# Kernel tuning notes

Measured on AMD Instinct MI355X. Metric: run time of the kernel, lower is better.

The kernel has to match this reference:

```python
import jax, jax.numpy as jnp
import numpy as np

B, N, D = 4, 2048, 1024
H = 8
DK = D // H            # 128, head qk dim (pre feature map)
DV = D // H            # 128, head v dim
DF = 2 * DK            # 256, hedgehog feature dim
CHUNK = 64
RMS_EPS = 1e-5


def setup_inputs() -> dict:
    key = jax.random.key(0)
    ks = jax.random.split(key, 10)
    s = D ** -0.5
    x = jax.random.normal(ks[0], (B, N, D), dtype=jnp.float32)
    Wq = jax.random.normal(ks[1], (D, D), dtype=jnp.float32) * s
    Wk = jax.random.normal(ks[2], (D, D), dtype=jnp.float32) * s
    Wv = jax.random.normal(ks[3], (D, D), dtype=jnp.float32) * s
    Wo = jax.random.normal(ks[4], (D, D), dtype=jnp.float32) * s
    eye = jnp.eye(DK, dtype=jnp.float32)
    # Hedgehog maps are initialized as identity; add small noise to exercise math
    fmq_w = eye + 0.02 * jax.random.normal(ks[5], (DK, DK), dtype=jnp.float32)
    fmq_b = 0.02 * jax.random.normal(ks[6], (DK,), dtype=jnp.float32)
    fmk_w = eye + 0.02 * jax.random.normal(ks[7], (DK, DK), dtype=jnp.float32)
    fmk_b = 0.02 * jax.random.normal(ks[8], (DK,), dtype=jnp.float32)
    rms_w = 1.0 + 0.1 * jax.random.normal(ks[9], (DV,), dtype=jnp.float32)
    return {"x": x, "Wq": Wq, "Wk": Wk, "Wv": Wv, "Wo": Wo,
            "fmq_w": fmq_w, "fmq_b": fmq_b, "fmk_w": fmk_w, "fmk_b": fmk_b,
            "rms_w": rms_w}


def _hedgehog(x, w, b):
    # x: [B,H,N,DK]; Linear then concat(exp(y), exp(-y)) -> [B,H,N,2*DK]
    y = jnp.einsum('bhnd,ed->bhne', x, w) + b
    return jnp.concatenate([jnp.exp(y), jnp.exp(-y)], axis=-1)


def _fused_chunk_linear_attn(q, k, v):
    # Causal linear attention via chunked recurrence.
    # q,k: [B,H,N,DF]; v: [B,H,N,DV]; q already scaled.
    b, h, n, df = q.shape
    dv = v.shape[-1]
    nc = n // CHUNK
    def to_chunks(t):
        d = t.shape[-1]
        return t.reshape(b, h, nc, CHUNK, d).transpose(2, 0, 1, 3, 4)  # [Nc,B,H,C,d]
    qc, kc, vc = to_chunks(q), to_chunks(k), to_chunks(v)
    mask = jnp.tril(jnp.ones((CHUNK, CHUNK), dtype=bool))

    def step(S, inp):
        qi, ki, vi = inp                                   # [B,H,C,*]
        attn = jnp.einsum('bhcd,bhed->bhce', qi, ki)       # intra-chunk scores
        attn = jnp.where(mask, attn, 0.0)                  # causal (inclusive)
        intra = jnp.einsum('bhce,bhev->bhcv', attn, vi)
        inter = jnp.einsum('bhcd,bhdv->bhcv', qi, S)       # past-chunk state
        S = S + jnp.einsum('bhcd,bhcv->bhdv', ki, vi)
        return S, intra + inter

    S0 = jnp.zeros((b, h, df, dv), dtype=q.dtype)
    _, oc = jax.lax.scan(step, S0, (qc, kc, vc))           # oc: [Nc,B,H,C,DV]
    return oc.transpose(1, 2, 0, 3, 4).reshape(b, h, n, dv)


def reference(x, Wq, Wk, Wv, Wo, fmq_w, fmq_b, fmk_w, fmk_b, rms_w):
    b, n, d = x.shape
    split = lambda t: t.reshape(b, n, H, -1).transpose(0, 2, 1, 3)  # b h n d
    q = split(x @ Wq.T)
    k = split(x @ Wk.T)
    v = split(x @ Wv.T)
    q = _hedgehog(q, fmq_w, fmq_b)          # [B,H,N,DF]
    k = _hedgehog(k, fmk_w, fmk_b)
    scale = q.shape[-1] ** -0.5             # fla default: feat_dim**-0.5
    o = _fused_chunk_linear_attn(q * scale, k, v)
    # RMSNorm over head_v_dim
    o = o * jax.lax.rsqrt(jnp.mean(o * o, axis=-1, keepdims=True) + RMS_EPS) * rms_w
    o = o.transpose(0, 2, 1, 3).reshape(b, n, H * DV)
    return o @ Wo.T
```

## Files before the change

### kernel.cpp

```cpp
#include <hip/hip_runtime.h>
#include <cstdint>
#include <cstddef>

#define DEV __device__ __forceinline__

typedef __attribute__((ext_vector_type(8))) short   short8;
typedef __attribute__((ext_vector_type(4))) short   sshort4;
typedef __attribute__((ext_vector_type(8))) __bf16  bf16x8;
typedef __attribute__((ext_vector_type(4))) float   f32x4;

typedef void as1_void __attribute__((address_space(1)));
typedef void as3_void __attribute__((address_space(3)));

DEV short f2b(float f) {
  unsigned u = __float_as_uint(f);
  unsigned r = (u + 0x7fffu + ((u >> 16) & 1u)) >> 16;
  return (short)r;
}
DEV float b2f(short s) {
  return __uint_as_float(((unsigned)(unsigned short)s) << 16);
}

DEV void gload16(const void* g, void* l) {
  __builtin_amdgcn_global_load_lds((as1_void*)g, (as3_void*)l, 16, 0, 0);
}

DEV bf16x8 ld8(const short* p) { return *reinterpret_cast<const bf16x8*>(p); }

DEV f32x4 mfma16(bf16x8 a, bf16x8 b, f32x4 c) {
  return __builtin_amdgcn_mfma_f32_16x16x32_bf16(a, b, c, 0, 0, 0);
}

__global__ void convert_kernel(const float* __restrict__ src, short* __restrict__ dst, int n) {
  int i = (blockIdx.x * 256 + threadIdx.x) * 8;
  if (i + 8 > n) return;
  float4 a = *(const float4*)(src + i);
  float4 b = *(const float4*)(src + i + 4);
  short8 o;
  o[0] = f2b(a.x); o[1] = f2b(a.y); o[2] = f2b(a.z); o[3] = f2b(a.w);
  o[4] = f2b(b.x); o[5] = f2b(b.y); o[6] = f2b(b.z); o[7] = f2b(b.w);
  *(short8*)(dst + i) = o;
}

__global__ void eff_weights2_kernel(const float* __restrict__ Wq, const float* __restrict__ Wk,
                                    const float* __restrict__ fmq_w, const float* __restrict__ fmk_w,
                                    short* __restrict__ Wcat)
{
  __shared__ float fm[16 * 128];
  const int blk = blockIdx.x;
  const int sel = blk >> 6, h = (blk >> 3) & 7, eg = blk & 7;
  const float* W   = sel ? Wk : Wq;
  const float* fmw = sel ? fmk_w : fmq_w;
  const int tid = threadIdx.x;
  const int e0 = eg * 16;
  for (int i = tid; i < 2048; i += 256) fm[i] = fmw[e0 * 128 + i];
  __syncthreads();
  float acc[16][4] = {};
  for (int d = 0; d < 128; d += 4) {
    f32x4 w0 = *(const f32x4*)(W + (size_t)(h * 128 + d + 0) * 1024 + tid * 4);
    f32x4 w1 = *(const f32x4*)(W + (size_t)(h * 128 + d + 1) * 1024 + tid * 4);
    f32x4 w2 = *(const f32x4*)(W + (size_t)(h * 128 + d + 2) * 1024 + tid * 4);
    f32x4 w3 = *(const f32x4*)(W + (size_t)(h * 128 + d + 3) * 1024 + tid * 4);
#pragma unroll
    for (int e = 0; e < 16; ++e) {
      f32x4 fv = *(const f32x4*)&fm[e * 128 + d];
#pragma unroll
      for (int c = 0; c < 4; ++c)
        acc[e][c] += fv[0] * w0[c] + fv[1] * w1[c] + fv[2] * w2[c] + fv[3] * w3[c];
    }
  }
#pragma unroll
  for (int e = 0; e < 16; ++e) {
    sshort4 o;
#pragma unroll
    for (int c = 0; c < 4; ++c) o[c] = f2b(acc[e][c]);
    *(sshort4*)(Wcat + (size_t)(sel * 1024 + h * 128 + e0 + e) * 1024 + tid * 4) = o;
  }
}

template<int EPI>
__launch_bounds__(512, 2)
__global__ void gemm256(const short* __restrict__ A, const short* __restrict__ B,
                        const int K, const int N, float* __restrict__ C,
                        const float* __restrict__ qb, const float* __restrict__ kb,
                        short* __restrict__ qf, short* __restrict__ kf,
                        short* __restrict__ kfT, short* __restrict__ vT)
{
  __shared__ __align__(16) short lds[65536];
  float* ep = (float*)lds;

  const int tid = threadIdx.x;
  const int w = tid >> 6, l = tid & 63;
  const int wr = w >> 2, wc = w & 3;

  const int nbx = gridDim.x;
  const int orig = blockIdx.y * nbx + blockIdx.x;
  const int cpx = (nbx * gridDim.y) >> 3;
  const int wg = (orig & 7) * cpx + (orig >> 3);
  const int m0 = (wg / nbx) * 256, n0 = (wg % nbx) * 256;

  const int srow = tid >> 3;
  const int scol = ((tid & 7) ^ (srow & 7)) * 8;
  const int wbase = w * 8;

  f32x4 acc[8][4] = {};

  auto STG = [&](const short* src, int g0, int p, int aoff, int R, int t) {
    gload16(src + (size_t)(g0 + R + srow) * K + t * 64 + scol,
            lds + p * 32768 + aoff + (R + wbase) * 64);
  };

#pragma unroll
  for (int R = 0; R < 256; R += 64) {
    STG(A, m0, 0, 0, R, 0);
    STG(B, n0, 0, 16384, R, 0);
    STG(A, m0, 1, 0, R, 1);
    STG(B, n0, 1, 16384, R, 1);
  }
  asm volatile("s_waitcnt vmcnt(0)" ::: "memory");
  __builtin_amdgcn_s_barrier();

#define PHASE(p, q, STAGES, TAIL) { \
    bf16x8 af[4][2], bf[2][2]; \
    _Pragma("unroll") \
    for (int m = 0; m < 4; ++m) { \
      const int r = wr * 128 + ((q) >> 1) * 64 + m * 16 + (l & 15); \
      _Pragma("unroll") \
      for (int kk = 0; kk < 2; ++kk) \
        af[m][kk] = ld8(lds + (p) * 32768 + r * 64 + ((kk * 4 + (l >> 4)) ^ (r & 7)) * 8); \
    } \
    _Pragma("unroll") \
    for (int n = 0; n < 2; ++n) { \
      const int r = wc * 64 + ((q) & 1) * 32 + n * 16 + (l & 15); \
      _Pragma("unroll") \
      for (int kk = 0; kk < 2; ++kk) \
        bf[n][kk] = ld8(lds + (p) * 32768 + 16384 + r * 64 + ((kk * 4 + (l >> 4)) ^ (r & 7)) * 8); \
    } \
    STAGES; \
    __builtin_amdgcn_s_barrier(); \
    asm volatile("s_waitcnt lgkmcnt(0)" ::: "memory"); \
    __builtin_amdgcn_sched_barrier(0); \
    __builtin_amdgcn_s_setprio(1); \
    _Pragma("unroll") \
    for (int m = 0; m < 4; ++m) \
      _Pragma("unroll") \
      for (int n = 0; n < 2; ++n) \
        _Pragma("unroll") \
        for (int kk = 0; kk < 2; ++kk) \
          acc[((q) >> 1) * 4 + m][((q) & 1) * 2 + n] = \
            mfma16(af[m][kk], bf[n][kk], acc[((q) >> 1) * 4 + m][((q) & 1) * 2 + n]); \
    __builtin_amdgcn_s_setprio(0); \
    TAIL; \
    __builtin_amdgcn_s_barrier(); \
  }

  const int NI = K >> 7;
  for (int i = 0; i < NI; ++i) {
    const int t1 = 2 * i + 1, t2 = 2 * i + 2, t3 = 2 * i + 3;
    const bool sE = (i < NI - 1), sL = (i > 0);
    PHASE(0, 0, {
      if (sL) { STG(A, m0, 1, 0, 64, t1); STG(A, m0, 1, 0, 192, t1);
                STG(B, n0, 1, 16384, 0, t1); STG(B, n0, 1, 16384, 64, t1); } }, {});
    PHASE(0, 1, {
      if (sL) { STG(B, n0, 1, 16384, 128, t1); STG(B, n0, 1, 16384, 192, t1); } }, {});
    PHASE(0, 2, {
      if (sE) { STG(A, m0, 0, 0, 0, t2); STG(A, m0, 0, 0, 128, t2); } }, {});
    PHASE(0, 3, {}, {
      if (i == NI - 1) { asm volatile("s_waitcnt vmcnt(0)" ::: "memory"); }
      else             { asm volatile("s_waitcnt vmcnt(2)" ::: "memory"); } });
    PHASE(1, 0, {
      if (sE) { STG(A, m0, 0, 0, 64, t2); STG(A, m0, 0, 0, 192, t2); } }, {});
    PHASE(1, 1, {
      if (sE) { STG(B, n0, 0, 16384, 0, t2); STG(B, n0, 0, 16384, 64, t2); } }, {});
    PHASE(1, 2, {
      if (sE) { STG(B, n0, 0, 16384, 128, t2); STG(B, n0, 0, 16384, 192, t2); } }, {});
    PHASE(1, 3, {
      if (sE) { STG(A, m0, 1, 0, 0, t3); STG(A, m0, 1, 0, 128, t3); } }, {
      asm volatile("s_waitcnt vmcnt(2)" ::: "memory"); });
  }
#undef PHASE

  const int seg = (EPI == 1) ? (n0 >> 10) : 0;
  const int b = m0 >> 11, tok0 = m0 & 2047, c0 = tok0 >> 6;
  const int hbase = (n0 & 1023) >> 7;
  const int bh0 = b * 8 + hbase;

#pragma unroll
  for (int h = 0; h < 4; ++h) {
    __syncthreads();
    if (wr == (h >> 1)) {
      const int mbase = (h & 1) * 4;
#pragma unroll
      for (int n = 0; n < 4; ++n) {
        const int cl = wc * 64 + n * 16 + (l & 15);
        float bb = 0.f;
        if constexpr (EPI == 1) bb = (seg == 0) ? qb[cl & 127] : (seg == 1) ? kb[cl & 127] : 0.f;
#pragma unroll
        for (int m4 = 0; m4 < 4; ++m4)
#pragma unroll
          for (int r = 0; r < 4; ++r) {
            const int rl = m4 * 16 + (l >> 4) * 4 + r;
            ep[rl * 264 + (cl ^ ((rl & 3) << 2))] = acc[mbase + m4][n][r] + bb;
          }
      }
    }
    __syncthreads();

    if constexpr (EPI == 0) {
#pragma unroll
      for (int it = 0; it < 8; ++it) {
        const int tl = it * 8 + (tid >> 6);
        const int cc4 = (tid & 63) * 4;
        f32x4 v4 = *(const f32x4*)&ep[tl * 264 + (cc4 ^ ((tl & 3) << 2))];
        *(f32x4*)(C + (size_t)(m0 + h * 64 + tl) * N + n0 + cc4) = v4;
      }
    } else {
      const int cc = c0 + h;
      if (seg <= 1) {
        short* dst = (seg == 0) ? qf : kf;
        const float sc = (seg == 0) ? 0.0625f : 1.0f;
#pragma unroll
        for (int it = 0; it < 8; ++it) {
          const int tl = it * 8 + (tid >> 6);
          const int cc4 = (tid & 63) * 4;
          f32x4 y4 = *(const f32x4*)&ep[tl * 264 + (cc4 ^ ((tl & 3) << 2))];
          sshort4 sp, sm;
#pragma unroll
          for (int j = 0; j < 4; ++j) {
            sp[j] = f2b(__expf(y4[j]) * sc);
            sm[j] = f2b(__expf(-y4[j]) * sc);
          }
          const int hh = cc4 >> 7, e = cc4 & 127;
          short* rowp = dst + ((size_t)(bh0 + hh) * 2048 + tok0 + h * 64 + tl) * 256;
          *(sshort4*)(rowp + e)       = sp;
          *(sshort4*)(rowp + 128 + e) = sm;
        }
        if (seg == 1) {
#pragma unroll
          for (int p2 = 0; p2 < 8; ++p2) {
            const int idx = p2 * 512 + tid;
            const int er = idx >> 3, oct = (idx & 7) * 8;
            const int hh = er >> 8, rr = er & 255, e = rr & 127, sg = rr >> 7;
            const int cgc = hh * 128 + e;
            short8 o;
#pragma unroll
            for (int ii = 0; ii < 8; ++ii) {
              float y = ep[(oct + ii) * 264 + (cgc ^ (((oct + ii) & 3) << 2))];
              o[ii] = f2b(__expf(sg ? -y : y));
            }
            *(short8*)(kfT + ((size_t)(bh0 + hh) * 32 + cc) * 16384 + (size_t)rr * 64 + oct) = o;
          }
        }
      } else {
#pragma unroll
        for (int p2 = 0; p2 < 4; ++p2) {
          const int idx = p2 * 512 + tid;
          const int er = idx >> 3, oct = (idx & 7) * 8;
          const int hh = er >> 7, vv = er & 127;
          short8 o;
#pragma unroll
          for (int ii = 0; ii < 8; ++ii)
            o[ii] = f2b(ep[(oct + ii) * 264 + (er ^ (((oct + ii) & 3) << 2))]);
          *(short8*)(vT + ((size_t)(bh0 + hh) * 32 + cc) * 8192 + (size_t)vv * 64 + oct) = o;
        }
      }
    }
  }
}

__launch_bounds__(256, 3)
__global__ void passA_kernel(const short* __restrict__ kfT, const short* __restrict__ vT,
                             short* __restrict__ GT)
{
  const int bhc = blockIdx.x;
  const int tid = threadIdx.x, w = tid >> 6, l = tid & 63;
  __shared__ __align__(16) short skT[256 * 64];
  __shared__ __align__(16) short svt[128 * 64];
  const short* kg = kfT + (size_t)bhc * 256 * 64;
  const short* vg = vT  + (size_t)bhc * 128 * 64;
  short* G = GT + (size_t)bhc * 128 * 256;
  const int sr8 = l >> 3, sl8 = ((l & 7) ^ sr8) * 8;

#pragma unroll
  for (int j = 0; j < 8; ++j) {
    const int seg = w * 8 + j;
    gload16(kg + (size_t)(seg * 8 + sr8) * 64 + sl8, skT + seg * 512);
  }
#pragma unroll
  for (int j = 0; j < 4; ++j) {
    const int seg = w * 4 + j;
    gload16(vg + (size_t)(seg * 8 + sr8) * 64 + sl8, svt + seg * 512);
  }
  __syncthreads();

#pragma unroll
  for (int mi = 0; mi < 2; ++mi) {
    const int v0 = w * 32 + mi * 16;
    bf16x8 a[2];
#pragma unroll
    for (int ks = 0; ks < 2; ++ks)
      a[ks] = ld8(svt + (v0 + (l & 15)) * 64 + ((ks * 4 + (l >> 4)) ^ (l & 7)) * 8);
    f32x4 acc[16] = {};
#pragma unroll
    for (int nt = 0; nt < 16; ++nt)
#pragma unroll
      for (int ks = 0; ks < 2; ++ks) {
        bf16x8 b = ld8(skT + (nt * 16 + (l & 15)) * 64 + ((ks * 4 + (l >> 4)) ^ (l & 7)) * 8);
        acc[nt] = mfma16(a[ks], b, acc[nt]);
      }
#pragma unroll
    for (int nt = 0; nt < 16; ++nt)
#pragma unroll
      for (int r = 0; r < 4; ++r)
        G[(v0 + (l >> 4) * 4 + r) * 256 + nt * 16 + (l & 15)] = f2b(acc[nt][r]);
  }
}

__global__ void prefix_kernel(short* __restrict__ GT) {
  const int bh = blockIdx.x >> 4, slab = blockIdx.x & 15;
  short* base = GT + (size_t)bh * 32 * 32768 + slab * 2048 + threadIdx.x * 8;
  float acc[8] = {};
  short8 g = *(const short8*)base;
  for (int c = 0; c < 32; ++c) {
    short* p = base + (size_t)c * 32768;
    short8 gn = {};
    if (c < 31) gn = *(const short8*)(p + 32768);
    short8 s;
#pragma unroll
    for (int j = 0; j < 8; ++j) s[j] = f2b(acc[j]);
    *(short8*)p = s;
#pragma unroll
    for (int j = 0; j < 8; ++j) acc[j] += b2f(g[j]);
    g = gn;
  }
}

__launch_bounds__(256, 3)
__global__ void passC_kernel(const short* __restrict__ qf, const short* __restrict__ kf,
                             const short* __restrict__ vT, const short* __restrict__ ST,
                             const float* __restrict__ rms_w, short* __restrict__ o_n)
{
  const int bhc = blockIdx.x, bh = bhc >> 5, c = bhc & 31;
  const int tid = threadIdx.x, w = tid >> 6, l = tid & 63;
  __shared__ __align__(16) short bufA[64 * 256];
  __shared__ __align__(16) short bufV[64 * 64];
  __shared__ __align__(16) short attn[64 * 72];
  const short* qg = qf + ((size_t)bh * 2048 + c * 64) * 256;
  const short* kg = kf + ((size_t)bh * 2048 + c * 64) * 256;
  const short* vg = vT + (size_t)bhc * 128 * 64;
  const short* sg = ST + (size_t)bhc * 128 * 256;
  const int r0 = w * 16;
  const int sr8 = l >> 3, sl8 = ((l & 7) ^ sr8) * 8;
  const int l5 = l >> 5, s32 = l & 31;

#pragma unroll
  for (int j = 0; j < 8; ++j) {
    const int seg = w * 8 + j;
    const int row = seg * 2 + l5;
    gload16(kg + (size_t)row * 256 + (s32 ^ (row & 7)) * 8, bufA + seg * 512);
  }
  bf16x8 qreg[8];
#pragma unroll
  for (int ks = 0; ks < 8; ++ks)
    qreg[ks] = ld8(qg + (size_t)(r0 + (l & 15)) * 256 + ks * 32 + (l >> 4) * 8);

  __syncthreads();
  f32x4 s[4] = {};
#pragma unroll
  for (int ks = 0; ks < 8; ++ks) {
    const int rs = ((ks * 4 + (l >> 4)) ^ (l & 7)) * 8;
#pragma unroll
    for (int nt = 0; nt < 4; ++nt)
      s[nt] = mfma16(qreg[ks], ld8(bufA + (nt * 16 + (l & 15)) * 256 + rs), s[nt]);
  }
#pragma unroll
  for (int nt = 0; nt < 4; ++nt)
#pragma unroll
    for (int r = 0; r < 4; ++r) {
      int rr = r0 + (l >> 4) * 4 + r;
      int tt = nt * 16 + (l & 15);
      attn[rr * 72 + tt] = (tt <= rr) ? f2b(s[nt][r]) : (short)0;
    }

  f32x4 o[8] = {};
#pragma unroll
  for (int h = 0; h < 2; ++h) {
    __syncthreads();
#pragma unroll
    for (int j = 0; j < 8; ++j) {
      const int seg = w * 8 + j;
      const int row = seg * 2 + l5;
      gload16(sg + (size_t)(h * 64 + row) * 256 + (s32 ^ (row & 7)) * 8, bufA + seg * 512);
    }
#pragma unroll
    for (int j = 0; j < 2; ++j) {
      const int seg = w * 2 + j;
      const int row = seg * 8 + sr8;
      gload16(vg + (size_t)(h * 64 + row) * 64 + sl8, bufV + seg * 512);
    }
    __syncthreads();
#pragma unroll
    for (int ks = 0; ks < 2; ++ks) {
      bf16x8 a = ld8(attn + (r0 + (l & 15)) * 72 + ks * 32 + (l >> 4) * 8);
      const int rs = ((ks * 4 + (l >> 4)) ^ (l & 7)) * 8;
#pragma unroll
      for (int nt = 0; nt < 4; ++nt)
        o[h * 4 + nt] = mfma16(a, ld8(bufV + (nt * 16 + (l & 15)) * 64 + rs), o[h * 4 + nt]);
    }
#pragma unroll
    for (int ks = 0; ks < 8; ++ks) {
      const int rs = ((ks * 4 + (l >> 4)) ^ (l & 7)) * 8;
#pragma unroll
      for (int nt = 0; nt < 4; ++nt)
        o[h * 4 + nt] = mfma16(qreg[ks], ld8(bufA + (nt * 16 + (l & 15)) * 256 + rs), o[h * 4 + nt]);
    }
  }

  const int b = bh >> 3, hh = bh & 7;
#pragma unroll
  for (int r = 0; r < 4; ++r) {
    float ss = 0.f;
#pragma unroll
    for (int nt = 0; nt < 8; ++nt) ss += o[nt][r] * o[nt][r];
    ss += __shfl_xor(ss, 1);
    ss += __shfl_xor(ss, 2);
    ss += __shfl_xor(ss, 4);
    ss += __shfl_xor(ss, 8);
    float sc = rsqrtf(ss * (1.0f / 128.0f) + 1e-5f);
    int tok = c * 64 + r0 + (l >> 4) * 4 + r;
    size_t ob = ((size_t)b * 2048 + tok) * 1024 + hh * 128;
#pragma unroll
    for (int nt = 0; nt < 8; ++nt) {
      int vcol = nt * 16 + (l & 15);
      o_n[ob + vcol] = f2b(o[nt][r] * sc * rms_w[vcol]);
    }
  }
}

extern "C" void kernel_launch(void* const* d_in, const int* in_sizes, int n_in,
                              void* d_out, int out_size, void* d_ws, size_t ws_size,
                              hipStream_t stream)
{
  const float* x     = (const float*)d_in[0];
  const float* Wq    = (const float*)d_in[1];
  const float* Wk    = (const float*)d_in[2];
  const float* Wv    = (const float*)d_in[3];
  const float* Wo    = (const float*)d_in[4];
  const float* fmq_w = (const float*)d_in[5];
  const float* fmq_b = (const float*)d_in[6];
  const float* fmk_w = (const float*)d_in[7];
  const float* fmk_b = (const float*)d_in[8];
  const float* rms_w = (const float*)d_in[9];
  float* out = (float*)d_out;

  char* ws = (char*)d_ws;
  short* x_b  = (short*)(ws);
  short* Wcat = (short*)(ws + 16777216);
  short* Wo_b = (short*)(ws + 23068672);
  short* qf   = (short*)(ws + 25165824);
  short* kf   = (short*)(ws + 58720256);
  short* kfT  = (short*)(ws + 92274688);
  short* vT   = (short*)(ws + 125829120);
  short* GT   = (short*)(ws + 142606336);
  short* o_n  = x_b;

  convert_kernel<<<4096, 256, 0, stream>>>(x, x_b, 8388608);
  convert_kernel<<<512, 256, 0, stream>>>(Wo, Wo_b, 1048576);
  convert_kernel<<<512, 256, 0, stream>>>(Wv, Wcat + 2097152, 1048576);
  eff_weights2_kernel<<<128, 256, 0, stream>>>(Wq, Wk, fmq_w, fmk_w, Wcat);
  gemm256<1><<<dim3(12, 32), 512, 0, stream>>>(x_b, Wcat, 1024, 3072, nullptr,
                                               fmq_b, fmk_b, qf, kf, kfT, vT);
  passA_kernel<<<1024, 256, 0, stream>>>(kfT, vT, GT);
  prefix_kernel<<<512, 256, 0, stream>>>(GT);
  passC_kernel<<<1024, 256, 0, stream>>>(qf, kf, vT, GT, rms_w, o_n);
  gemm256<0><<<dim3(4, 32), 512, 0, stream>>>(o_n, Wo_b, 1024, 1024, out,
                                              nullptr, nullptr, nullptr, nullptr,
                                              nullptr, nullptr);
}
```

Measured before the change: 363.3 us.

## Merge prep kernels into one launch and reuse GEMM LDS fragments across phases

```diff
diff --git a/kernel.cpp b/kernel.cpp
--- a/kernel.cpp
+++ b/kernel.cpp
@@ -31,50 +31,58 @@
   return __builtin_amdgcn_mfma_f32_16x16x32_bf16(a, b, c, 0, 0, 0);
 }
 
-__global__ void convert_kernel(const float* __restrict__ src, short* __restrict__ dst, int n) {
-  int i = (blockIdx.x * 256 + threadIdx.x) * 8;
-  if (i + 8 > n) return;
-  float4 a = *(const float4*)(src + i);
-  float4 b = *(const float4*)(src + i + 4);
-  short8 o;
-  o[0] = f2b(a.x); o[1] = f2b(a.y); o[2] = f2b(a.z); o[3] = f2b(a.w);
-  o[4] = f2b(b.x); o[5] = f2b(b.y); o[6] = f2b(b.z); o[7] = f2b(b.w);
-  *(short8*)(dst + i) = o;
-}
-
-__global__ void eff_weights2_kernel(const float* __restrict__ Wq, const float* __restrict__ Wk,
-                                    const float* __restrict__ fmq_w, const float* __restrict__ fmk_w,
-                                    short* __restrict__ Wcat)
+__global__ void prep_kernel(const float* __restrict__ x, const float* __restrict__ Wo,
+                            const float* __restrict__ Wq, const float* __restrict__ Wk,
+                            const float* __restrict__ Wv,
+                            const float* __restrict__ fmq_w, const float* __restrict__ fmk_w,
+                            short* __restrict__ x_b, short* __restrict__ Wo_b,
+                            short* __restrict__ Wcat)
 {
-  __shared__ float fm[16 * 128];
   const int blk = blockIdx.x;
-  const int sel = blk >> 6, h = (blk >> 3) & 7, eg = blk & 7;
-  const float* W   = sel ? Wk : Wq;
-  const float* fmw = sel ? fmk_w : fmq_w;
   const int tid = threadIdx.x;
-  const int e0 = eg * 16;
-  for (int i = tid; i < 2048; i += 256) fm[i] = fmw[e0 * 128 + i];
-  __syncthreads();
-  float acc[16][4] = {};
-  for (int d = 0; d < 128; d += 4) {
-    f32x4 w0 = *(const f32x4*)(W + (size_t)(h * 128 + d + 0) * 1024 + tid * 4);
-    f32x4 w1 = *(const f32x4*)(W + (size_t)(h * 128 + d + 1) * 1024 + tid * 4);
-    f32x4 w2 = *(const f32x4*)(W + (size_t)(h * 128 + d + 2) * 1024 + tid * 4);
-    f32x4 w3 = *(const f32x4*)(W + (size_t)(h * 128 + d + 3) * 1024 + tid * 4);
+  if (blk < 5120) {
+    const float* src;
+    short* dst;
+    int i;
+    if (blk < 4096)      { src = x;  dst = x_b;            i = (blk * 256 + tid) * 8; }
+    else if (blk < 4608) { src = Wo; dst = Wo_b;           i = ((blk - 4096) * 256 + tid) * 8; }
+    else                 { src = Wv; dst = Wcat + 2097152; i = ((blk - 4608) * 256 + tid) * 8; }
+    float4 a = *(const float4*)(src + i);
+    float4 b = *(const float4*)(src + i + 4);
+    short8 o;
+    o[0] = f2b(a.x); o[1] = f2b(a.y); o[2] = f2b(a.z); o[3] = f2b(a.w);
+    o[4] = f2b(b.x); o[5] = f2b(b.y); o[6] = f2b(b.z); o[7] = f2b(b.w);
+    *(short8*)(dst + i) = o;
+  } else {
+    __shared__ float fm[16 * 128];
+    const int eb = blk - 5120;
+    const int sel = eb >> 6, h = (eb >> 3) & 7, eg = eb & 7;
+    const float* W   = sel ? Wk : Wq;
+    const float* fmw = sel ? fmk_w : fmq_w;
+    const int e0 = eg * 16;
+    for (int i = tid; i < 2048; i += 256) fm[i] = fmw[e0 * 128 + i];
+    __syncthreads();
+    float acc[16][4] = {};
+    for (int d = 0; d < 128; d += 4) {
+      f32x4 w0 = *(const f32x4*)(W + (size_t)(h * 128 + d + 0) * 1024 + tid * 4);
+      f32x4 w1 = *(const f32x4*)(W + (size_t)(h * 128 + d + 1) * 1024 + tid * 4);
+      f32x4 w2 = *(const f32x4*)(W + (size_t)(h * 128 + d + 2) * 1024 + tid * 4);
+      f32x4 w3 = *(const f32x4*)(W + (size_t)(h * 128 + d + 3) * 1024 + tid * 4);
+#pragma unroll
+      for (int e = 0; e < 16; ++e) {
+        f32x4 fv = *(const f32x4*)&fm[e * 128 + d];
+#pragma unroll
+        for (int c = 0; c < 4; ++c)
+          acc[e][c] += fv[0] * w0[c] + fv[1] * w1[c] + fv[2] * w2[c] + fv[3] * w3[c];
+      }
+    }
 #pragma unroll
     for (int e = 0; e < 16; ++e) {
-      f32x4 fv = *(const f32x4*)&fm[e * 128 + d];
-#pragma unroll
-      for (int c = 0; c < 4; ++c)
-        acc[e][c] += fv[0] * w0[c] + fv[1] * w1[c] + fv[2] * w2[c] + fv[3] * w3[c];
-    }
-  }
-#pragma unroll
-  for (int e = 0; e < 16; ++e) {
-    sshort4 o;
-#pragma unroll
-    for (int c = 0; c < 4; ++c) o[c] = f2b(acc[e][c]);
-    *(sshort4*)(Wcat + (size_t)(sel * 1024 + h * 128 + e0 + e) * 1024 + tid * 4) = o;
+      sshort4 o;
+#pragma unroll
+      for (int c = 0; c < 4; ++c) o[c] = f2b(acc[e][c]);
+      *(sshort4*)(Wcat + (size_t)(sel * 1024 + h * 128 + e0 + e) * 1024 + tid * 4) = o;
+    }
   }
 }
 
@@ -104,6 +112,8 @@
   const int wbase = w * 8;
 
   f32x4 acc[8][4] = {};
+  bf16x8 af[4][2];
+  bf16x8 bg[2][2][2];
 
   auto STG = [&](const short* src, int g0, int p, int aoff, int R, int t) {
     gload16(src + (size_t)(g0 + R + srow) * K + t * 64 + scol,
@@ -120,21 +130,24 @@
   asm volatile("s_waitcnt vmcnt(0)" ::: "memory");
   __builtin_amdgcn_s_barrier();
 
-#define PHASE(p, q, STAGES, TAIL) { \
-    bf16x8 af[4][2], bf[2][2]; \
-    _Pragma("unroll") \
-    for (int m = 0; m < 4; ++m) { \
-      const int r = wr * 128 + ((q) >> 1) * 64 + m * 16 + (l & 15); \
+#define PHASE(p, q, DOLDA, DOLDB, STAGES, TAIL) { \
+    if (DOLDA) { \
       _Pragma("unroll") \
-      for (int kk = 0; kk < 2; ++kk) \
-        af[m][kk] = ld8(lds + (p) * 32768 + r * 64 + ((kk * 4 + (l >> 4)) ^ (r & 7)) * 8); \
+      for (int m = 0; m < 4; ++m) { \
+        const int r = wr * 128 + ((q) >> 1) * 64 + m * 16 + (l & 15); \
+        _Pragma("unroll") \
+        for (int kk = 0; kk < 2; ++kk) \
+          af[m][kk] = ld8(lds + (p) * 32768 + r * 64 + ((kk * 4 + (l >> 4)) ^ (r & 7)) * 8); \
+      } \
     } \
-    _Pragma("unroll") \
-    for (int n = 0; n < 2; ++n) { \
-      const int r = wc * 64 + ((q) & 1) * 32 + n * 16 + (l & 15); \
+    if (DOLDB) { \
       _Pragma("unroll") \
-      for (int kk = 0; kk < 2; ++kk) \
-        bf[n][kk] = ld8(lds + (p) * 32768 + 16384 + r * 64 + ((kk * 4 + (l >> 4)) ^ (r & 7)) * 8); \
+      for (int n = 0; n < 2; ++n) { \
+        const int r = wc * 64 + ((q) & 1) * 32 + n * 16 + (l & 15); \
+        _Pragma("unroll") \
+        for (int kk = 0; kk < 2; ++kk) \
+          bg[(q) & 1][n][kk] = ld8(lds + (p) * 32768 + 16384 + r * 64 + ((kk * 4 + (l >> 4)) ^ (r & 7)) * 8); \
+      } \
     } \
     STAGES; \
     __builtin_amdgcn_s_barrier(); \
@@ -148,7 +161,7 @@
         _Pragma("unroll") \
         for (int kk = 0; kk < 2; ++kk) \
           acc[((q) >> 1) * 4 + m][((q) & 1) * 2 + n] = \
-            mfma16(af[m][kk], bf[n][kk], acc[((q) >> 1) * 4 + m][((q) & 1) * 2 + n]); \
+            mfma16(af[m][kk], bg[(q) & 1][n][kk], acc[((q) >> 1) * 4 + m][((q) & 1) * 2 + n]); \
     __builtin_amdgcn_s_setprio(0); \
     TAIL; \
     __builtin_amdgcn_s_barrier(); \
@@ -158,23 +171,23 @@
   for (int i = 0; i < NI; ++i) {
     const int t1 = 2 * i + 1, t2 = 2 * i + 2, t3 = 2 * i + 3;
     const bool sE = (i < NI - 1), sL = (i > 0);
-    PHASE(0, 0, {
+    PHASE(0, 0, 1, 1, {
       if (sL) { STG(A, m0, 1, 0, 64, t1); STG(A, m0, 1, 0, 192, t1);
                 STG(B, n0, 1, 16384, 0, t1); STG(B, n0, 1, 16384, 64, t1); } }, {});
-    PHASE(0, 1, {
+    PHASE(0, 1, 0, 1, {
       if (sL) { STG(B, n0, 1, 16384, 128, t1); STG(B, n0, 1, 16384, 192, t1); } }, {});
-    PHASE(0, 2, {
+    PHASE(0, 2, 1, 0, {
       if (sE) { STG(A, m0, 0, 0, 0, t2); STG(A, m0, 0, 0, 128, t2); } }, {});
-    PHASE(0, 3, {}, {
+    PHASE(0, 3, 0, 0, {}, {
       if (i == NI - 1) { asm volatile("s_waitcnt vmcnt(0)" ::: "memory"); }
       else             { asm volatile("s_waitcnt vmcnt(2)" ::: "memory"); } });
-    PHASE(1, 0, {
+    PHASE(1, 0, 1, 1, {
       if (sE) { STG(A, m0, 0, 0, 64, t2); STG(A, m0, 0, 0, 192, t2); } }, {});
-    PHASE(1, 1, {
+    PHASE(1, 1, 0, 1, {
       if (sE) { STG(B, n0, 0, 16384, 0, t2); STG(B, n0, 0, 16384, 64, t2); } }, {});
-    PHASE(1, 2, {
+    PHASE(1, 2, 1, 0, {
       if (sE) { STG(B, n0, 0, 16384, 128, t2); STG(B, n0, 0, 16384, 192, t2); } }, {});
-    PHASE(1, 3, {
+    PHASE(1, 3, 0, 0, {
       if (sE) { STG(A, m0, 1, 0, 0, t3); STG(A, m0, 1, 0, 128, t3); } }, {
       asm volatile("s_waitcnt vmcnt(2)" ::: "memory"); });
   }
@@ -464,10 +477,8 @@
   short* GT   = (short*)(ws + 142606336);
   short* o_n  = x_b;
 
-  convert_kernel<<<4096, 256, 0, stream>>>(x, x_b, 8388608);
-  convert_kernel<<<512, 256, 0, stream>>>(Wo, Wo_b, 1048576);
-  convert_kernel<<<512, 256, 0, stream>>>(Wv, Wcat + 2097152, 1048576);
-  eff_weights2_kernel<<<128, 256, 0, stream>>>(Wq, Wk, fmq_w, fmk_w, Wcat);
+  prep_kernel<<<5248, 256, 0, stream>>>(x, Wo, Wq, Wk, Wv, fmq_w, fmk_w,
+                                        x_b, Wo_b, Wcat);
   gemm256<1><<<dim3(12, 32), 512, 0, stream>>>(x_b, Wcat, 1024, 3072, nullptr,
                                                fmq_b, fmk_b, qf, kf, kfT, vT);
   passA_kernel<<<1024, 256, 0, stream>>>(kfT, vT, GT);
```

Measured after the change: 355.3 us. 2.2% less time.
